# Performance work log

Hardware: AMD Instinct MI355X
Metric: run time of the kernel (lower is better)

## Reference

```python
import jax, jax.numpy as jnp
import numpy as np

N_NODES = 50000
N_EDGES = 800000
DIM_NODE = 64
DIM_EDGE = 32
OUT_DIM = 64
NEG_SLOPE = 0.01  # torch F.leaky_relu default; module's negative_slope arg is unused in forward


def setup_inputs() -> dict:
    key = jax.random.key(0)
    k = jax.random.split(key, 8)
    d_in1 = 2 * DIM_NODE + DIM_EDGE  # 160
    d_h = 2 * DIM_NODE               # 128
    # Kaiming-uniform-ish init scale like torch Linear
    def lin(kw, kb, fan_in, fan_out):
        bound = 1.0 / np.sqrt(fan_in)
        W = jax.random.uniform(kw, (fan_out, fan_in), minval=-bound, maxval=bound, dtype=jnp.float32)
        b = jax.random.uniform(kb, (fan_out,), minval=-bound, maxval=bound, dtype=jnp.float32)
        return W, b
    W1, b1 = lin(k[0], k[1], d_in1, d_h)
    W2, b2 = lin(k[2], k[3], d_h, OUT_DIM)
    x = jax.random.normal(k[4], (N_NODES, DIM_NODE), dtype=jnp.float32)
    edge_index = jax.random.randint(k[5], (2, N_EDGES), 0, N_NODES, dtype=jnp.int64 if jax.config.jax_enable_x64 else jnp.int32).astype(jnp.int32)
    edge_attr = jax.random.normal(k[6], (N_EDGES, DIM_EDGE), dtype=jnp.float32)
    return {"x": x, "edge_index": edge_index, "edge_attr": edge_attr,
            "W1": W1, "b1": b1, "W2": W2, "b2": b2}


def reference(x, edge_index, edge_attr, W1, b1, W2, b2):
    # gather endpoint node features per edge: [E, dim_node]
    x_i = x[edge_index[0]]
    x_j = x[edge_index[1]]
    mask = jnp.concatenate([x_i, x_j, edge_attr], axis=-1)  # [E, 2*dn+de]
    h = jnp.dot(mask, W1.T) + b1                             # [E, 2*dn]
    h = jnp.where(h >= 0, h, NEG_SLOPE * h)                  # leaky_relu (slope 0.01)
    out = jnp.dot(h, W2.T) + b2                              # [E, out_dim]
    return out
```

## Files before the change

### kernel.cpp

```cpp
#include <hip/hip_runtime.h>
#include <stdint.h>
#include <stddef.h>


typedef short short8 __attribute__((ext_vector_type(8)));
typedef float f32x4 __attribute__((ext_vector_type(4)));

__device__ __forceinline__ short f2bf(float f) {
  union { float f; unsigned u; } v; v.f = f;
  unsigned r = (v.u + 0x7fffu + ((v.u >> 16) & 1u)) >> 16;
  return (short)r;
}

__device__ __forceinline__ short8 cvt8(const float* __restrict__ p) {
  f32x4 a = *(const f32x4*)p;
  f32x4 b = *(const f32x4*)(p + 4);
  short8 r;
  r[0] = f2bf(a[0]); r[1] = f2bf(a[1]); r[2] = f2bf(a[2]); r[3] = f2bf(a[3]);
  r[4] = f2bf(b[0]); r[5] = f2bf(b[1]); r[6] = f2bf(b[2]); r[7] = f2bf(b[3]);
  return r;
}

__global__ __launch_bounds__(256, 2)
void edge_mlp(const float* __restrict__ x, const int* __restrict__ ei,
              const float* __restrict__ ea, const float* __restrict__ W1,
              const float* __restrict__ b1, const float* __restrict__ W2,
              const float* __restrict__ b2, float* __restrict__ out,
              int E, int ntiles)
{
  __shared__ short sW1[128 * 168];
  __shared__ short sH[4][32 * 40];

  const int tid  = threadIdx.x;
  const int lane = tid & 63;
  const int wave = tid >> 6;
  const int m    = lane & 15;
  const int quad = lane >> 4;

  for (int i = tid; i < 128 * 160; i += 256) {
    int n = i / 160;
    int k = i - n * 160;
    sW1[n * 168 + k] = f2bf(W1[i]);
  }

  short8 w2f[4][4];
#pragma unroll
  for (int ot = 0; ot < 4; ++ot)
#pragma unroll
    for (int c = 0; c < 4; ++c)
      w2f[ot][c] = cvt8(W2 + (size_t)(ot * 16 + m) * 128 + c * 32 + quad * 8);

  float b1v[8], b2v[4];
#pragma unroll
  for (int nt = 0; nt < 8; ++nt) b1v[nt] = b1[nt * 16 + m];
#pragma unroll
  for (int ot = 0; ot < 4; ++ot) b2v[ot] = b2[ot * 16 + m];

  __syncthreads();

  short* sHw = sH[wave];

  for (int t = blockIdx.x; t < ntiles; t += gridDim.x) {
    const int ebase = t * 128 + wave * 32;

    short8 a1[2][5];
#pragma unroll
    for (int mt = 0; mt < 2; ++mt) {
      int e = ebase + mt * 16 + m;
      e = (e < E) ? e : (E - 1);
      const int i0 = ei[e];
      const int i1 = ei[E + e];
      const float* r0 = x + (size_t)i0 * 64 + quad * 8;
      const float* r1 = x + (size_t)i1 * 64 + quad * 8;
      a1[mt][0] = cvt8(r0);
      a1[mt][1] = cvt8(r0 + 32);
      a1[mt][2] = cvt8(r1);
      a1[mt][3] = cvt8(r1 + 32);
      a1[mt][4] = cvt8(ea + (size_t)e * 32 + quad * 8);
    }

    f32x4 acc2[2][4];
#pragma unroll
    for (int mt = 0; mt < 2; ++mt)
#pragma unroll
      for (int ot = 0; ot < 4; ++ot) {
        f32x4 z = { b2v[ot], b2v[ot], b2v[ot], b2v[ot] };
        acc2[mt][ot] = z;
      }

#pragma unroll
    for (int c = 0; c < 4; ++c) {
#pragma unroll
      for (int sub = 0; sub < 2; ++sub) {
        const int nt = c * 2 + sub;
        f32x4 h0 = { b1v[nt], b1v[nt], b1v[nt], b1v[nt] };
        f32x4 h1 = h0;
#pragma unroll
        for (int kt = 0; kt < 5; ++kt) {
          short8 bf = *(const short8*)&sW1[(nt * 16 + m) * 168 + kt * 32 + quad * 8];
          h0 = __builtin_amdgcn_mfma_f32_16x16x32_bf16(a1[0][kt], bf, h0, 0, 0, 0);
          h1 = __builtin_amdgcn_mfma_f32_16x16x32_bf16(a1[1][kt], bf, h1, 0, 0, 0);
        }
#pragma unroll
        for (int r = 0; r < 4; ++r) {
          float v0 = h0[r]; v0 = (v0 >= 0.0f) ? v0 : 0.01f * v0;
          float v1 = h1[r]; v1 = (v1 >= 0.0f) ? v1 : 0.01f * v1;
          sHw[(quad * 4 + r) * 40 + sub * 16 + m]      = f2bf(v0);
          sHw[(16 + quad * 4 + r) * 40 + sub * 16 + m] = f2bf(v1);
        }
      }
#pragma unroll
      for (int mt = 0; mt < 2; ++mt) {
        short8 a2 = *(const short8*)&sHw[(mt * 16 + m) * 40 + quad * 8];
#pragma unroll
        for (int ot = 0; ot < 4; ++ot)
          acc2[mt][ot] = __builtin_amdgcn_mfma_f32_16x16x32_bf16(a2, w2f[ot][c], acc2[mt][ot], 0, 0, 0);
      }
    }

#pragma unroll
    for (int mt = 0; mt < 2; ++mt)
#pragma unroll
      for (int ot = 0; ot < 4; ++ot)
#pragma unroll
        for (int r = 0; r < 4; ++r) {
          int er = ebase + mt * 16 + quad * 4 + r;
          if (er < E) out[(size_t)er * 64 + ot * 16 + m] = acc2[mt][ot][r];
        }
  }
}

extern "C" void kernel_launch(void* const* d_in, const int* in_sizes, int n_in,
                              void* d_out, int out_size, void* d_ws, size_t ws_size,
                              hipStream_t stream) {
  const float* x  = (const float*)d_in[0];
  const int*   ei = (const int*)d_in[1];
  const float* ea = (const float*)d_in[2];
  const float* W1 = (const float*)d_in[3];
  const float* b1 = (const float*)d_in[4];
  const float* W2 = (const float*)d_in[5];
  const float* b2 = (const float*)d_in[6];
  float* out = (float*)d_out;

  const int E = in_sizes[1] / 2;
  const int ntiles = (E + 127) / 128;
  int grid = ntiles < 1250 ? ntiles : 1250;

  edge_mlp<<<grid, 256, 0, stream>>>(x, ei, ea, W1, b1, W2, b2, out, E, ntiles);
}
```

Before: 386.8 us.

## Pre-convert node features to bf16 and use 512-thread blocks

Adds a pre-pass kernel that converts the node feature table to bf16 in workspace, so the per-edge gathers read half the bytes and skip the per-load conversion. The main kernel grows to 512 threads (8 waves, 256 edges per tile) with a grid of 512 persistent blocks, which spreads the shared W1 staging across more waves. This costs an extra kernel launch plus a full pass over x, and needs a workspace, with a fallback path when none is available. Registers are now capped by the 512x4 launch bound, so spills are possible.

```diff
diff --git a/kernel.cpp b/kernel.cpp
--- a/kernel.cpp
+++ b/kernel.cpp
@@ -21,15 +21,22 @@
   return r;
 }
 
-__global__ __launch_bounds__(256, 2)
-void edge_mlp(const float* __restrict__ x, const int* __restrict__ ei,
-              const float* __restrict__ ea, const float* __restrict__ W1,
-              const float* __restrict__ b1, const float* __restrict__ W2,
-              const float* __restrict__ b2, float* __restrict__ out,
-              int E, int ntiles)
+__global__ __launch_bounds__(256)
+void cvt_x_kernel(const float* __restrict__ x, short* __restrict__ xb, int n8) {
+  int i = blockIdx.x * blockDim.x + threadIdx.x;
+  if (i < n8) *(short8*)(xb + (size_t)i * 8) = cvt8(x + (size_t)i * 8);
+}
+
+template <bool XB>
+__global__ __launch_bounds__(512, 4)
+void edge_mlp(const float* __restrict__ x, const short* __restrict__ xb,
+              const int* __restrict__ ei, const float* __restrict__ ea,
+              const float* __restrict__ W1, const float* __restrict__ b1,
+              const float* __restrict__ W2, const float* __restrict__ b2,
+              float* __restrict__ out, int E, int ntiles)
 {
   __shared__ short sW1[128 * 168];
-  __shared__ short sH[4][32 * 40];
+  __shared__ short sH[8][32 * 40];
 
   const int tid  = threadIdx.x;
   const int lane = tid & 63;
@@ -37,7 +44,7 @@
   const int m    = lane & 15;
   const int quad = lane >> 4;
 
-  for (int i = tid; i < 128 * 160; i += 256) {
+  for (int i = tid; i < 128 * 160; i += 512) {
     int n = i / 160;
     int k = i - n * 160;
     sW1[n * 168 + k] = f2bf(W1[i]);
@@ -61,7 +68,7 @@
   short* sHw = sH[wave];
 
   for (int t = blockIdx.x; t < ntiles; t += gridDim.x) {
-    const int ebase = t * 128 + wave * 32;
+    const int ebase = t * 256 + wave * 32;
 
     short8 a1[2][5];
 #pragma unroll
@@ -70,12 +77,21 @@
       e = (e < E) ? e : (E - 1);
       const int i0 = ei[e];
       const int i1 = ei[E + e];
-      const float* r0 = x + (size_t)i0 * 64 + quad * 8;
-      const float* r1 = x + (size_t)i1 * 64 + quad * 8;
-      a1[mt][0] = cvt8(r0);
-      a1[mt][1] = cvt8(r0 + 32);
-      a1[mt][2] = cvt8(r1);
-      a1[mt][3] = cvt8(r1 + 32);
+      if constexpr (XB) {
+        const short* r0 = xb + (size_t)i0 * 64 + quad * 8;
+        const short* r1 = xb + (size_t)i1 * 64 + quad * 8;
+        a1[mt][0] = *(const short8*)r0;
+        a1[mt][1] = *(const short8*)(r0 + 32);
+        a1[mt][2] = *(const short8*)r1;
+        a1[mt][3] = *(const short8*)(r1 + 32);
+      } else {
+        const float* r0 = x + (size_t)i0 * 64 + quad * 8;
+        const float* r1 = x + (size_t)i1 * 64 + quad * 8;
+        a1[mt][0] = cvt8(r0);
+        a1[mt][1] = cvt8(r0 + 32);
+        a1[mt][2] = cvt8(r1);
+        a1[mt][3] = cvt8(r1 + 32);
+      }
       a1[mt][4] = cvt8(ea + (size_t)e * 32 + quad * 8);
     }
 
@@ -142,9 +158,20 @@
   const float* b2 = (const float*)d_in[6];
   float* out = (float*)d_out;
 
-  const int E = in_sizes[1] / 2;
-  const int ntiles = (E + 127) / 128;
-  int grid = ntiles < 1250 ? ntiles : 1250;
+  const int E  = in_sizes[1] / 2;
+  const int nx = in_sizes[0];
+  const int ntiles = (E + 255) / 256;
+  int grid = ntiles < 512 ? ntiles : 512;
 
-  edge_mlp<<<grid, 256, 0, stream>>>(x, ei, ea, W1, b1, W2, b2, out, E, ntiles);
+  short* xb = (short*)d_ws;
+  const bool usebf = (d_ws != nullptr) && (ws_size >= (size_t)nx * sizeof(short))
+                     && ((nx & 7) == 0);
+  if (usebf) {
+    const int n8 = nx / 8;
+    const int cg = (n8 + 255) / 256;
+    cvt_x_kernel<<<cg, 256, 0, stream>>>(x, xb, n8);
+    edge_mlp<true><<<grid, 512, 0, stream>>>(x, xb, ei, ea, W1, b1, W2, b2, out, E, ntiles);
+  } else {
+    edge_mlp<false><<<grid, 512, 0, stream>>>(x, nullptr, ei, ea, W1, b1, W2, b2, out, E, ntiles);
+  }
 }
```

New measurement: 459.0 us. +18.7%, slower.
